# Performance work log

Measured on AMD Instinct MI355X. Metric: run time of the kernel, lower is better.

Reference implementation:

```python
import jax, jax.numpy as jnp
import numpy as np

NUM_EMBEDDINGS = 1024
EMBEDDING_DIM = 256
E_LOSS_WEIGHT = 0.25
MU = 0.01
EPSILON = 1e-05
N_TOKENS = 65536


def setup_inputs() -> dict:
    key = jax.random.key(0)
    k1, k2, k3 = jax.random.split(key, 3)
    return {
        "inputs": jax.random.normal(k1, (N_TOKENS, EMBEDDING_DIM), dtype=jnp.float32),
        "embedding_weight": jax.random.normal(k2, (NUM_EMBEDDINGS, EMBEDDING_DIM), dtype=jnp.float32),
        "ema_w": jax.random.normal(k3, (NUM_EMBEDDINGS, EMBEDDING_DIM), dtype=jnp.float32),
        "ema_cluster_size": jnp.zeros((NUM_EMBEDDINGS,), dtype=jnp.float32),
    }


def reference(inputs, embedding_weight, ema_w, ema_cluster_size):
    N, D = inputs.shape
    K = embedding_weight.shape[0]

    # Squared L2 distances: [N, K]
    distances = (
        jnp.sum(inputs ** 2, axis=1, keepdims=True)
        + jnp.sum(embedding_weight ** 2, axis=1)
        - 2.0 * (inputs @ embedding_weight.T)
    )
    idx = jnp.argmin(distances, axis=1)              # [N]

    # Gather codebook entries (replaces one-hot @ weight)
    quantized_raw = embedding_weight[idx]            # [N, D]

    # Commitment loss (quantized detached)
    e_latent_loss = jnp.mean((jax.lax.stop_gradient(quantized_raw) - inputs) ** 2)
    loss = E_LOSS_WEIGHT * e_latent_loss

    # Per-code counts and scatter-sum of inputs (replaces one-hot matmuls)
    counts = jax.ops.segment_sum(jnp.ones((N,), inputs.dtype), idx, num_segments=K)  # [K]
    dw = jax.ops.segment_sum(inputs, idx, num_segments=K)                             # [K, D]

    # EMA updates (training branch)
    new_cluster = ema_cluster_size * (1.0 - MU) + MU * counts
    n = jnp.sum(new_cluster)
    new_cluster = (new_cluster + EPSILON) / (n + K * EPSILON) * n
    new_ema_w = ema_w * (1.0 - MU) + MU * dw
    new_embedding = new_ema_w / new_cluster[:, None]

    # Straight-through estimator
    quantized = inputs + jax.lax.stop_gradient(quantized_raw - inputs)

    avg_probs = counts / N
    perplexity = jnp.exp(-jnp.sum(avg_probs * jnp.log(avg_probs + 1e-10)))

    encoding_indices = idx.reshape(N, 1)
    return quantized, loss, encoding_indices, perplexity, new_cluster, new_ema_w, new_embedding
```

## Files before the change

### kernel.cpp

```cpp
#include <hip/hip_runtime.h>

typedef _Float16 half8 __attribute__((ext_vector_type(8)));
typedef _Float16 half4 __attribute__((ext_vector_type(4)));
typedef float f32x4 __attribute__((ext_vector_type(4)));

#define N_TOK 65536
#define DIM   256
#define KCODE 1024
#define MU_C  0.01f
#define EPS_C 1e-5f

#define O_Q    0
#define O_LOSS 16777216
#define O_IDX  16777217
#define O_PERP 16842753
#define O_NC   16842754
#define O_NEW  16843778
#define O_EMB  17105922

#define W_IDX   0
#define W_CNT   65536
#define W_CUR   66560
#define W_OFF   67584
#define W_CNTF  68608
#define W_NFLAG 69632
#define W_FLAG  69696
#define W_ORDER 135232
#define W_DW    200768
#define W_WSQ   462912
#define W_WH    463936
#define W_XSQF  595008
#define W_ELATA 660544
#define W_PACK  676928
#define W_HALF  808000

__device__ __forceinline__ int imin(int a, int b) { return a < b ? a : b; }
__device__ __forceinline__ int imax(int a, int b) { return a > b ? a : b; }

__global__ void k_init(const float* __restrict__ W, _Float16* __restrict__ Wh,
                       float* __restrict__ wsq, unsigned* __restrict__ wsu) {
    int gid = blockIdx.x * 256 + threadIdx.x;
    if (gid < 4097) wsu[W_CNT + gid] = 0u;
    ((float4*)(wsu + W_DW))[gid] = make_float4(0.f, 0.f, 0.f, 0.f);
    ((unsigned long long*)(wsu + W_PACK))[gid] = ~0ull;
    int row = gid >> 6, lane = gid & 63;
    float4 v = *(const float4*)(W + (size_t)row * 256 + lane * 4);
    half4 h;
    h[0] = (_Float16)v.x; h[1] = (_Float16)v.y; h[2] = (_Float16)v.z; h[3] = (_Float16)v.w;
    *(half4*)(Wh + (size_t)row * 256 + lane * 4) = h;
    float s = v.x * v.x + v.y * v.y + v.z * v.z + v.w * v.w;
#pragma unroll
    for (int off = 1; off < 64; off <<= 1) s += __shfl_xor(s, off);
    if (lane == 0) wsq[row] = s;
}

__global__ __launch_bounds__(256, 2) void argmin_mfma(
    const float* __restrict__ X, const _Float16* __restrict__ Wh,
    const float* __restrict__ wsq, unsigned long long* __restrict__ halfres)
{
    __shared__ _Float16 Bs[2][32 * 256];

    const int tid  = threadIdx.x;
    const int lane = tid & 63;
    const int w    = tid >> 6;
    const int l15  = lane & 15;
    const int lk   = lane >> 4;
    const int half  = blockIdx.x & 1;
    const int cbase = half * 512;
    const int t0    = (blockIdx.x >> 1) * 256;

    half8 a[4][8];
#pragma unroll
    for (int g2 = 0; g2 < 4; ++g2) {
        const float* xr = X + (size_t)(t0 + w * 64 + g2 * 16 + l15) * 256 + lk * 8;
#pragma unroll
        for (int g = 0; g < 8; ++g) {
            float4 u0 = *(const float4*)(xr + g * 32);
            float4 u1 = *(const float4*)(xr + g * 32 + 4);
            half8 h;
            h[0] = (_Float16)u0.x; h[1] = (_Float16)u0.y;
            h[2] = (_Float16)u0.z; h[3] = (_Float16)u0.w;
            h[4] = (_Float16)u1.x; h[5] = (_Float16)u1.y;
            h[6] = (_Float16)u1.z; h[7] = (_Float16)u1.w;
            a[g2][g] = h;
        }
    }

    int u1a[16], u2a[16];
#pragma unroll
    for (int i = 0; i < 16; ++i) { u1a[i] = 0x7FFFFFFF; u2a[i] = 0x7FFFFFFF; }

#define STAGE(cc, bb)                                                          \
    _Pragma("unroll")                                                          \
    for (int i = 0; i < 4; ++i) {                                              \
        int loff = (w * 4 + i) * 1024;                                         \
        int off  = loff + lane * 16;                                           \
        int row  = off >> 9;                                                   \
        int slot = (off >> 4) & 31;                                            \
        const _Float16* src = Wh + (size_t)(cbase + (cc) * 32 + row) * 256     \
                                 + ((slot ^ row) << 3);                        \
        __builtin_amdgcn_global_load_lds(                                      \
            (const __attribute__((address_space(1))) void*)src,                \
            (__attribute__((address_space(3))) void*)((char*)Bs[bb] + loff),   \
            16, 0, 0);                                                         \
    }

    STAGE(0, 0);

    for (int c = 0; c < 16; ++c) {
        const int cur = c & 1;
        if (c < 15) {
            STAGE(c + 1, cur ^ 1);
            asm volatile("s_waitcnt vmcnt(4)" ::: "memory");
        } else {
            asm volatile("s_waitcnt vmcnt(0)" ::: "memory");
        }
        __builtin_amdgcn_s_barrier();

        f32x4 acc[4][2];
#pragma unroll
        for (int g2 = 0; g2 < 4; ++g2) { acc[g2][0] = (f32x4)0.0f; acc[g2][1] = (f32x4)0.0f; }

        __builtin_amdgcn_s_setprio(1);
#pragma unroll
        for (int ks = 0; ks < 8; ++ks) {
            const int j = ks * 4 + lk;
            const char* base = (const char*)Bs[cur];
            half8 b0 = *(const half8*)(base + l15 * 512        + ((j ^ l15) << 4));
            half8 b1 = *(const half8*)(base + (16 + l15) * 512 + ((j ^ (16 + l15)) << 4));
#pragma unroll
            for (int g2 = 0; g2 < 4; ++g2) {
                acc[g2][0] = __builtin_amdgcn_mfma_f32_16x16x32_f16(
                    a[g2][ks], b0, acc[g2][0], 0, 0, 0);
                acc[g2][1] = __builtin_amdgcn_mfma_f32_16x16x32_f16(
                    a[g2][ks], b1, acc[g2][1], 0, 0, 0);
            }
        }
        __builtin_amdgcn_s_setprio(0);

#pragma unroll
        for (int nf = 0; nf < 2; ++nf) {
            int   code = cbase + c * 32 + nf * 16 + l15;
            float tc   = fmaf(0.5f, wsq[code], 512.0f);
#pragma unroll
            for (int g2 = 0; g2 < 4; ++g2)
#pragma unroll
                for (int r = 0; r < 4; ++r) {
                    float sv = tc - acc[g2][nf][r];
                    int u = (__float_as_int(sv) & 0xFFFFFC00) | code;
                    int s = g2 * 4 + r;
                    u2a[s] = imin(u2a[s], imax(u1a[s], u));
                    u1a[s] = imin(u1a[s], u);
                }
        }
        __builtin_amdgcn_s_barrier();
    }
#undef STAGE

#pragma unroll
    for (int s = 0; s < 16; ++s) {
#pragma unroll
        for (int off = 1; off < 16; off <<= 1) {
            int b1 = __shfl_xor(u1a[s], off);
            int b2 = __shfl_xor(u2a[s], off);
            int n2 = imin(imin(u2a[s], b2), imax(u1a[s], b1));
            u1a[s] = imin(u1a[s], b1);
            u2a[s] = n2;
        }
    }
    if (l15 == 0) {
#pragma unroll
        for (int s = 0; s < 16; ++s) {
            int row = t0 + w * 64 + (s >> 2) * 16 + lk * 4 + (s & 3);
            halfres[(size_t)half * 65536 + row] =
                ((unsigned long long)(unsigned)u1a[s] << 32) | (unsigned)u2a[s];
        }
    }
}

__global__ void merge_halves(const unsigned long long* __restrict__ halfres,
                             int* __restrict__ idx_out, float* __restrict__ out,
                             unsigned* __restrict__ cnt,
                             unsigned* __restrict__ nflag, int* __restrict__ flaglist)
{
    int t = blockIdx.x * 256 + threadIdx.x;
    unsigned long long A = halfres[t], B = halfres[65536 + t];
    int a1 = (int)(A >> 32), a2 = (int)(unsigned)A;
    int b1 = (int)(B >> 32), b2 = (int)(unsigned)B;
    int u1 = imin(a1, b1);
    int u2 = imin(imax(a1, b1), imin(a2, b2));
    int code = u1 & 1023;
    idx_out[t] = code;
    out[O_IDX + t] = (float)code;
    atomicAdd(&cnt[code], 1u);
    float s1 = __int_as_float(u1 & 0xFFFFFC00);
    float s2 = __int_as_float(u2 & 0xFFFFFC00);
    if (s2 - s1 < 0.125f) {
        unsigned p = atomicAdd(nflag, 1u);
        flaglist[p] = t;
    }
}

__global__ void cleanup_xsq(const float* __restrict__ X,
                            const unsigned* __restrict__ nflagp,
                            const int* __restrict__ flaglist,
                            float* __restrict__ xsqf) {
    int n = (int)nflagp[0];
    int wid  = (blockIdx.x * 256 + threadIdx.x) >> 6;
    int lane = threadIdx.x & 63;
    for (int i = wid; i < n; i += 1024) {
        const float* row = X + (size_t)flaglist[i] * 256;
        float4 v = *(const float4*)(row + lane * 4);
        float s = v.x * v.x + v.y * v.y + v.z * v.z + v.w * v.w;
#pragma unroll
        for (int off = 1; off < 64; off <<= 1) s += __shfl_xor(s, off);
        if (lane == 0) xsqf[i] = s;
    }
}

__global__ __launch_bounds__(256, 2) void cleanup_gemm(
    const float* __restrict__ X, const float* __restrict__ W,
    const float* __restrict__ wsq, const unsigned* __restrict__ nflagp,
    const int* __restrict__ flaglist, const float* __restrict__ xsqf,
    unsigned long long* __restrict__ pack)
{
    __shared__ float xs [16][64];
    __shared__ float wps[16][128];
    __shared__ float wsq_s[128];

    const int n = (int)nflagp[0];
    const int tid = threadIdx.x;
    const int tx  = tid & 15;
    const int ty  = tid >> 4;
    const int c0    = (blockIdx.x & 7) * 128;
    const int tslot = blockIdx.x >> 3;
    const int srow_x = tid & 63,  sq_x = tid >> 6;
    const int srow_w = tid & 127, sh_w = tid >> 7;

    if (tid < 128) wsq_s[tid] = wsq[c0 + tid];

    for (int tile = tslot; tile * 64 < n; tile += 256) {
        const int t0 = tile * 64;
        const int gtok = flaglist[imin(t0 + srow_x, n - 1)];
        const float* xrow = X + (size_t)gtok * DIM;
        const float* wrow = W + (size_t)(c0 + srow_w) * DIM + sh_w * 8;

        float xsq_r[4];
#pragma unroll
        for (int i = 0; i < 4; ++i) xsq_r[i] = xsqf[imin(t0 + ty * 4 + i, n - 1)];

        float minv[4]; int mini[4];
#pragma unroll
        for (int i = 0; i < 4; ++i) { minv[i] = 3.402823466e+38f; mini[i] = 0; }

        float acc[4][8];
#pragma unroll
        for (int i = 0; i < 4; ++i)
#pragma unroll
            for (int j = 0; j < 8; ++j) acc[i][j] = 0.0f;

        float4 xa = *(const float4*)(xrow + sq_x * 4);
        float4 wa = *(const float4*)(wrow);
        float4 wb = *(const float4*)(wrow + 4);

        for (int ks = 0; ks < 16; ++ks) {
            __syncthreads();
            xs[sq_x * 4 + 0][srow_x] = xa.x; xs[sq_x * 4 + 1][srow_x] = xa.y;
            xs[sq_x * 4 + 2][srow_x] = xa.z; xs[sq_x * 4 + 3][srow_x] = xa.w;
            wps[sh_w * 8 + 0][srow_w] = wa.x; wps[sh_w * 8 + 1][srow_w] = wa.y;
            wps[sh_w * 8 + 2][srow_w] = wa.z; wps[sh_w * 8 + 3][srow_w] = wa.w;
            wps[sh_w * 8 + 4][srow_w] = wb.x; wps[sh_w * 8 + 5][srow_w] = wb.y;
            wps[sh_w * 8 + 6][srow_w] = wb.z; wps[sh_w * 8 + 7][srow_w] = wb.w;
            __syncthreads();
            if (ks < 15) {
                xa = *(const float4*)(xrow + (ks + 1) * 16 + sq_x * 4);
                wa = *(const float4*)(wrow + (ks + 1) * 16);
                wb = *(const float4*)(wrow + (ks + 1) * 16 + 4);
            }
#pragma unroll
            for (int kl = 0; kl < 16; ++kl) {
                float4 av = *(const float4*)&xs [kl][ty * 4];
                float4 b0 = *(const float4*)&wps[kl][tx * 8];
                float4 b1 = *(const float4*)&wps[kl][tx * 8 + 4];
                float aa[4] = {av.x, av.y, av.z, av.w};
                float bb[8] = {b0.x, b0.y, b0.z, b0.w, b1.x, b1.y, b1.z, b1.w};
#pragma unroll
                for (int i = 0; i < 4; ++i)
#pragma unroll
                    for (int j = 0; j < 8; ++j)
                        acc[i][j] = fmaf(aa[i], bb[j], acc[i][j]);
            }
        }
#pragma unroll
        for (int i = 0; i < 4; ++i) {
#pragma unroll
            for (int j = 0; j < 8; ++j) {
                float t1 = xsq_r[i] + wsq_s[tx * 8 + j];
                float s  = t1 - 2.0f * acc[i][j];
                int   cc = c0 + tx * 8 + j;
                if (s < minv[i]) { minv[i] = s; mini[i] = cc; }
            }
        }
#pragma unroll
        for (int i = 0; i < 4; ++i) {
#pragma unroll
            for (int off = 1; off < 16; off <<= 1) {
                float ov = __shfl_xor(minv[i], off);
                int   oi = __shfl_xor(mini[i], off);
                if (ov < minv[i] || (ov == minv[i] && oi < mini[i])) {
                    minv[i] = ov; mini[i] = oi;
                }
            }
        }
        if (tx == 0) {
#pragma unroll
            for (int i = 0; i < 4; ++i) {
                int pos = t0 + ty * 4 + i;
                if (pos < n) {
                    unsigned long long pu =
                        ((unsigned long long)(unsigned)__float_as_int(minv[i]) << 32)
                        | (unsigned)mini[i];
                    atomicMin(&pack[pos], pu);
                }
            }
        }
        __syncthreads();
    }
}

__global__ void cleanup_write(const unsigned* __restrict__ nflagp,
                              const int* __restrict__ flaglist,
                              const unsigned long long* __restrict__ pack,
                              int* __restrict__ idx_out, float* __restrict__ out,
                              unsigned* __restrict__ cnt) {
    int n = (int)nflagp[0];
    for (int i = blockIdx.x * 256 + threadIdx.x; i < n; i += 65536) {
        int t = flaglist[i];
        int code = (int)(pack[i] & 0xFFFFFFFFull);
        int old  = idx_out[t];
        if (code != old) {
            idx_out[t] = code;
            out[O_IDX + t] = (float)code;
            atomicAdd(&cnt[code], 1u);
            atomicAdd(&cnt[old], 0xFFFFFFFFu);
        }
    }
}

__global__ __launch_bounds__(256) void k_scatter(
    const int* __restrict__ idx, const unsigned* __restrict__ cnt,
    unsigned* __restrict__ cursor, unsigned* __restrict__ order,
    float* __restrict__ cntf)
{
    __shared__ unsigned soffs[1024];
    __shared__ unsigned wsum[4];
    int t = threadIdx.x, lane = t & 63, wid = t >> 6;
    uint4 v = ((const uint4*)cnt)[t];
    if (blockIdx.x == 0) {
        cntf[4 * t + 0] = (float)v.x; cntf[4 * t + 1] = (float)v.y;
        cntf[4 * t + 2] = (float)v.z; cntf[4 * t + 3] = (float)v.w;
    }
    unsigned s = v.x + v.y + v.z + v.w;
    unsigned ps = s;
#pragma unroll
    for (int off = 1; off < 64; off <<= 1) {
        unsigned o = __shfl_up(ps, off);
        if (lane >= off) ps += o;
    }
    if (lane == 63) wsum[wid] = ps;
    __syncthreads();
    unsigned base = 0;
#pragma unroll
    for (int i = 0; i < 4; ++i) if (i < wid) base += wsum[i];
    unsigned excl = base + ps - s;
    soffs[4 * t + 0] = excl;
    soffs[4 * t + 1] = excl + v.x;
    soffs[4 * t + 2] = excl + v.x + v.y;
    soffs[4 * t + 3] = excl + v.x + v.y + v.z;
    __syncthreads();
    int tok = blockIdx.x * 256 + threadIdx.x;
    int c = idx[tok];
    unsigned p = atomicAdd(&cursor[c], 1u);
    order[soffs[c] + p] = ((unsigned)c << 16) | (unsigned)tok;
}

__global__ __launch_bounds__(256) void k_epilogue_dw(
    const float* __restrict__ X, const float* __restrict__ W,
    const unsigned* __restrict__ order, float* __restrict__ out,
    float* __restrict__ dw, float* __restrict__ elat_arr)
{
    int gw   = (blockIdx.x * 256 + threadIdx.x) >> 6;
    int lane = threadIdx.x & 63;
    int p0 = gw * 16;
    float4 acc = make_float4(0.f, 0.f, 0.f, 0.f);
    float4 wreg = make_float4(0.f, 0.f, 0.f, 0.f);
    int cur = -1;
    float e = 0.f;
#pragma unroll 4
    for (int i = 0; i < 16; ++i) {
        unsigned u = order[p0 + i];
        int t = (int)(u & 0xFFFFu), c = (int)(u >> 16);
        float4 x4 = *(const float4*)(X + (size_t)t * 256 + lane * 4);
        if (c != cur) {
            if (cur >= 0) {
                float* dwp = dw + (size_t)cur * 256 + lane * 4;
                atomicAdd(dwp + 0, acc.x); atomicAdd(dwp + 1, acc.y);
                atomicAdd(dwp + 2, acc.z); atomicAdd(dwp + 3, acc.w);
            }
            wreg = *(const float4*)(W + (size_t)c * 256 + lane * 4);
            cur = c; acc = x4;
        } else {
            acc.x += x4.x; acc.y += x4.y; acc.z += x4.z; acc.w += x4.w;
        }
        ((float4*)(out + O_Q))[(size_t)t * 64 + lane] = wreg;
        float d0 = wreg.x - x4.x, d1 = wreg.y - x4.y;
        float d2 = wreg.z - x4.z, d3 = wreg.w - x4.w;
        e += d0 * d0 + d1 * d1 + d2 * d2 + d3 * d3;
    }
    if (cur >= 0) {
        float* dwp = dw + (size_t)cur * 256 + lane * 4;
        atomicAdd(dwp + 0, acc.x); atomicAdd(dwp + 1, acc.y);
        atomicAdd(dwp + 2, acc.z); atomicAdd(dwp + 3, acc.w);
    }
#pragma unroll
    for (int off = 1; off < 64; off <<= 1) e += __shfl_xor(e, off);
    __shared__ float se[4];
    int wid = threadIdx.x >> 6;
    if (lane == 0) se[wid] = e;
    __syncthreads();
    if (threadIdx.x == 0) elat_arr[blockIdx.x] = se[0] + se[1] + se[2] + se[3];
}

__global__ __launch_bounds__(1024) void finalize_small(
    const float* __restrict__ ecs, const float* __restrict__ counts,
    const float* __restrict__ elat_arr, float* __restrict__ out)
{
    int k = threadIdx.x;
    float cnt = counts[k];
    float nc = ecs[k] * (1.0f - MU_C) + MU_C * cnt;
    float p = cnt * (1.0f / 65536.0f);
    float h = p * logf(p + 1e-10f);
    float el = elat_arr[k];
    float rn = nc, rh = h, re = el;
#pragma unroll
    for (int off = 1; off < 64; off <<= 1) {
        rn += __shfl_xor(rn, off);
        rh += __shfl_xor(rh, off);
        re += __shfl_xor(re, off);
    }
    __shared__ float sn[16], sh[16], sef[16];
    int wid = k >> 6, lane = k & 63;
    if (lane == 0) { sn[wid] = rn; sh[wid] = rh; sef[wid] = re; }
    __syncthreads();
    float n = 0.0f, H = 0.0f, E = 0.0f;
#pragma unroll
    for (int i = 0; i < 16; ++i) { n += sn[i]; H += sh[i]; E += sef[i]; }
    out[O_NC + k] = (nc + EPS_C) / (n + 1024.0f * EPS_C) * n;
    if (k == 0) {
        out[O_LOSS] = 0.25f * (E * (1.0f / 16777216.0f));
        out[O_PERP] = expf(-H);
    }
}

__global__ void finalize_embed(const float* __restrict__ ema_w,
                               const float* __restrict__ dw, float* __restrict__ out)
{
    int gid = blockIdx.x * blockDim.x + threadIdx.x;
    int k = gid >> 8;
    float ew = ema_w[gid] * (1.0f - MU_C) + MU_C * dw[gid];
    out[O_NEW + gid] = ew;
    out[O_EMB + gid] = ew / out[O_NC + k];
}

extern "C" void kernel_launch(void* const* d_in, const int* in_sizes, int n_in,
                              void* d_out, int out_size, void* d_ws, size_t ws_size,
                              hipStream_t stream) {
    const float* X     = (const float*)d_in[0];
    const float* W     = (const float*)d_in[1];
    const float* ema_w = (const float*)d_in[2];
    const float* ecs   = (const float*)d_in[3];
    float*    out    = (float*)d_out;
    unsigned* wsu    = (unsigned*)d_ws;
    float*    wsf    = (float*)d_ws;
    int*      idx    = (int*)d_ws + W_IDX;
    unsigned* cnt    = wsu + W_CNT;
    unsigned* cursor = wsu + W_CUR;
    float*    cntf   = wsf + W_CNTF;
    unsigned* nflag  = wsu + W_NFLAG;
    int*      flags  = (int*)d_ws + W_FLAG;
    unsigned* order  = wsu + W_ORDER;
    float*    dw     = wsf + W_DW;
    float*    wsq    = wsf + W_WSQ;
    _Float16* Wh     = (_Float16*)(wsu + W_WH);
    float*    xsqf   = wsf + W_XSQF;
    float*    elatA  = wsf + W_ELATA;
    unsigned long long* pack    = (unsigned long long*)(wsu + W_PACK);
    unsigned long long* halfres = (unsigned long long*)(wsu + W_HALF);

    hipLaunchKernelGGL(k_init,         dim3(256),   dim3(256),  0, stream, W, Wh, wsq, wsu);
    hipLaunchKernelGGL(argmin_mfma,    dim3(512),   dim3(256),  0, stream, X, Wh, wsq, halfres);
    hipLaunchKernelGGL(merge_halves,   dim3(256),   dim3(256),  0, stream, halfres, idx, out, cnt, nflag, flags);
    hipLaunchKernelGGL(cleanup_xsq,    dim3(256),   dim3(256),  0, stream, X, nflag, flags, xsqf);
    hipLaunchKernelGGL(cleanup_gemm,   dim3(2048),  dim3(256),  0, stream, X, W, wsq, nflag, flags, xsqf, pack);
    hipLaunchKernelGGL(cleanup_write,  dim3(256),   dim3(256),  0, stream, nflag, flags, pack, idx, out, cnt);
    hipLaunchKernelGGL(k_scatter,      dim3(256),   dim3(256),  0, stream, idx, cnt, cursor, order, cntf);
    hipLaunchKernelGGL(k_epilogue_dw,  dim3(1024),  dim3(256),  0, stream, X, W, order, out, dw, elatA);
    hipLaunchKernelGGL(finalize_small, dim3(1),     dim3(1024), 0, stream, ecs, cntf, elatA, out);
    hipLaunchKernelGGL(finalize_embed, dim3(1024),  dim3(256),  0, stream, ema_w, dw, out);
}
```

Measured before the change: 210.4 us.

## Software-pipeline MFMA chunks with argmin epilogue using double accumulators

Splits each codebook chunk's work into an MFMA phase and an argmin epilogue, and uses two accumulator sets so the epilogue of chunk c-1 is issued after the MFMAs of chunk c. The aim is to let the VALU min/max work overlap with in-flight matrix instructions instead of waiting on the MFMA results right away. It also drops the explicit accumulator zeroing by feeding zero into the first MFMA. The cost is another 32 accumulator VGPRs, which may lower occupancy or cause spills.

Result: slower. 240.7 us (+14.4%).

```diff
diff --git a/kernel.cpp b/kernel.cpp
--- a/kernel.cpp
+++ b/kernel.cpp
@@ -90,6 +90,9 @@
 #pragma unroll
     for (int i = 0; i < 16; ++i) { u1a[i] = 0x7FFFFFFF; u2a[i] = 0x7FFFFFFF; }
 
+    const f32x4 Z = (f32x4)0.0f;
+    f32x4 accA[4][2], accB[4][2];
+
 #define STAGE(cc, bb)                                                          \
     _Pragma("unroll")                                                          \
     for (int i = 0; i < 4; ++i) {                                              \
@@ -105,57 +108,66 @@
             16, 0, 0);                                                         \
     }
 
+#define CHUNK(cc, ACC)                                                         \
+    {                                                                          \
+        const int cur_ = (cc) & 1;                                             \
+        if ((cc) < 15) {                                                       \
+            STAGE((cc) + 1, cur_ ^ 1);                                         \
+            asm volatile("s_waitcnt vmcnt(4)" ::: "memory");                   \
+        } else {                                                               \
+            asm volatile("s_waitcnt vmcnt(0)" ::: "memory");                   \
+        }                                                                      \
+        __builtin_amdgcn_s_barrier();                                          \
+        __builtin_amdgcn_s_setprio(1);                                         \
+        _Pragma("unroll")                                                      \
+        for (int ks = 0; ks < 8; ++ks) {                                       \
+            const int j = ks * 4 + lk;                                         \
+            const char* base_ = (const char*)Bs[cur_];                         \
+            half8 b0 = *(const half8*)(base_ + l15 * 512 + ((j ^ l15) << 4));  \
+            half8 b1 = *(const half8*)(base_ + (16 + l15) * 512                \
+                                        + ((j ^ (16 + l15)) << 4));            \
+            _Pragma("unroll")                                                  \
+            for (int g2 = 0; g2 < 4; ++g2) {                                   \
+                ACC[g2][0] = __builtin_amdgcn_mfma_f32_16x16x32_f16(           \
+                    a[g2][ks], b0, ks ? ACC[g2][0] : Z, 0, 0, 0);              \
+                ACC[g2][1] = __builtin_amdgcn_mfma_f32_16x16x32_f16(           \
+                    a[g2][ks], b1, ks ? ACC[g2][1] : Z, 0, 0, 0);              \
+            }                                                                  \
+        }                                                                      \
+        __builtin_amdgcn_s_setprio(0);                                         \
+        __builtin_amdgcn_s_barrier();                                          \
+    }
+
+#define EPI(cc, ACC)                                                           \
+    _Pragma("unroll")                                                          \
+    for (int nf = 0; nf < 2; ++nf) {                                           \
+        int   code = cbase + (cc) * 32 + nf * 16 + l15;                        \
+        float tc   = fmaf(0.5f, wsq[code], 512.0f);                            \
+        _Pragma("unroll")                                                      \
+        for (int g2 = 0; g2 < 4; ++g2)                                         \
+            _Pragma("unroll")                                                  \
+            for (int r = 0; r < 4; ++r) {                                      \
+                float sv = tc - ACC[g2][nf][r];                                \
+                int u = (__float_as_int(sv) & 0xFFFFFC00) | code;              \
+                int s = g2 * 4 + r;                                            \
+                u2a[s] = imin(u2a[s], imax(u1a[s], u));                        \
+                u1a[s] = imin(u1a[s], u);                                      \
+            }                                                                  \
+    }
+
     STAGE(0, 0);
 
-    for (int c = 0; c < 16; ++c) {
-        const int cur = c & 1;
-        if (c < 15) {
-            STAGE(c + 1, cur ^ 1);
-            asm volatile("s_waitcnt vmcnt(4)" ::: "memory");
-        } else {
-            asm volatile("s_waitcnt vmcnt(0)" ::: "memory");
-        }
-        __builtin_amdgcn_s_barrier();
-
-        f32x4 acc[4][2];
-#pragma unroll
-        for (int g2 = 0; g2 < 4; ++g2) { acc[g2][0] = (f32x4)0.0f; acc[g2][1] = (f32x4)0.0f; }
-
-        __builtin_amdgcn_s_setprio(1);
-#pragma unroll
-        for (int ks = 0; ks < 8; ++ks) {
-            const int j = ks * 4 + lk;
-            const char* base = (const char*)Bs[cur];
-            half8 b0 = *(const half8*)(base + l15 * 512        + ((j ^ l15) << 4));
-            half8 b1 = *(const half8*)(base + (16 + l15) * 512 + ((j ^ (16 + l15)) << 4));
-#pragma unroll
-            for (int g2 = 0; g2 < 4; ++g2) {
-                acc[g2][0] = __builtin_amdgcn_mfma_f32_16x16x32_f16(
-                    a[g2][ks], b0, acc[g2][0], 0, 0, 0);
-                acc[g2][1] = __builtin_amdgcn_mfma_f32_16x16x32_f16(
-                    a[g2][ks], b1, acc[g2][1], 0, 0, 0);
-            }
-        }
-        __builtin_amdgcn_s_setprio(0);
-
-#pragma unroll
-        for (int nf = 0; nf < 2; ++nf) {
-            int   code = cbase + c * 32 + nf * 16 + l15;
-            float tc   = fmaf(0.5f, wsq[code], 512.0f);
-#pragma unroll
-            for (int g2 = 0; g2 < 4; ++g2)
-#pragma unroll
-                for (int r = 0; r < 4; ++r) {
-                    float sv = tc - acc[g2][nf][r];
-                    int u = (__float_as_int(sv) & 0xFFFFFC00) | code;
-                    int s = g2 * 4 + r;
-                    u2a[s] = imin(u2a[s], imax(u1a[s], u));
-                    u1a[s] = imin(u1a[s], u);
-                }
-        }
-        __builtin_amdgcn_s_barrier();
-    }
+    for (int c2 = 0; c2 < 16; c2 += 2) {
+        CHUNK(c2, accA);
+        if (c2 > 0) { EPI(c2 - 1, accB); }
+        CHUNK(c2 + 1, accB);
+        EPI(c2, accA);
+    }
+    EPI(15, accB);
+
 #undef STAGE
+#undef CHUNK
+#undef EPI
 
 #pragma unroll
     for (int s = 0; s < 16; ++s) {
```
